# Kernel tuning notes

Hardware: AMD Instinct MI355X
Metric: run time of the kernel (lower is better)

Reference implementation:

```python
import jax, jax.numpy as jnp
import numpy as np
from jax import lax

CLASSES = 6
R = 8            # zoom_factor
FEAT = 32        # DUC loops i,j in range(32)
OUT_PAD = 304    # DUC hardcodes zeros(b,6,304,304)
IMG = 256        # original image H=W -> final bilinear resize target
BN_EPS = 1e-5
DN = ('NCHW', 'OIHW', 'NCHW')


def _duc(x):
    # x: [B, classes*r*r, H', W'] ; original loop only reads top-left 32x32
    x = x[:, :, :FEAT, :FEAT]
    B = x.shape[0]
    # channel order in original: view(b, classes, r*r) -> (classes, r, r)
    y = x.reshape(B, CLASSES, R, R, FEAT, FEAT)
    y = y.transpose(0, 1, 4, 2, 5, 3).reshape(B, CLASSES, FEAT * R, FEAT * R)  # [B,6,256,256]
    pad = OUT_PAD - FEAT * R
    return jnp.pad(y, ((0, 0), (0, 0), (0, pad), (0, pad)))  # zeros ring like torch.zeros buffer


def _bilinear_align_corners(x, oh, ow):
    b, c, h, w = x.shape
    ys = jnp.linspace(0.0, h - 1.0, oh)
    xs = jnp.linspace(0.0, w - 1.0, ow)
    y0 = jnp.floor(ys).astype(jnp.int32)
    x0 = jnp.floor(xs).astype(jnp.int32)
    y1 = jnp.minimum(y0 + 1, h - 1)
    x1 = jnp.minimum(x0 + 1, w - 1)
    wy = (ys - y0)[None, None, :, None]
    wx = (xs - x0)[None, None, None, :]
    rows = x[:, :, y0, :] * (1.0 - wy) + x[:, :, y1, :] * wy          # [b,c,oh,w]
    out = rows[:, :, :, x0] * (1.0 - wx) + rows[:, :, :, x1] * wx     # [b,c,oh,ow]
    return out


def setup_inputs() -> dict:
    key = jax.random.key(0)
    ks = jax.random.split(key, 8)
    x = jax.random.normal(ks[0], (16, 5632, 32, 32), jnp.float32)
    w1 = jax.random.normal(ks[1], (512, 5632, 1, 1), jnp.float32) * 0.02
    gamma = 1.0 + 0.1 * jax.random.normal(ks[2], (512,), jnp.float32)
    beta = 0.1 * jax.random.normal(ks[3], (512,), jnp.float32)
    mean = 0.1 * jax.random.normal(ks[4], (512,), jnp.float32)
    var = jax.random.uniform(ks[5], (512,), jnp.float32, 0.5, 1.5)
    w2 = jax.random.normal(ks[6], (CLASSES * R * R, 512, 1, 1), jnp.float32) * 0.02
    b2 = jax.random.normal(ks[7], (CLASSES * R * R,), jnp.float32) * 0.02
    return {'x': x, 'w1': w1, 'gamma': gamma, 'beta': beta, 'mean': mean, 'var': var, 'w2': w2, 'b2': b2}


def reference(x, w1, gamma, beta, mean, var, w2, b2):
    # cls head: 1x1 conv with padding=1 (quirk in source) -> 34x34 map
    h = lax.conv_general_dilated(x, w1, (1, 1), ((1, 1), (1, 1)), dimension_numbers=DN)
    inv = lax.rsqrt(var + BN_EPS)
    h = (h - mean[None, :, None, None]) * (inv * gamma)[None, :, None, None] + beta[None, :, None, None]
    h = jax.nn.relu(h)  # Dropout2d is identity at inference
    h = lax.conv_general_dilated(h, w2, (1, 1), ((0, 0), (0, 0)), dimension_numbers=DN)
    h = h + b2[None, :, None, None]            # [B,384,34,34]
    h = _duc(h)                                # [B,6,304,304]
    h = jax.nn.softmax(h, axis=1)
    return _bilinear_align_corners(h, IMG, IMG)  # [B,6,256,256]
```

## Files before the change

### kernel.cpp

```cpp
#include <hip/hip_runtime.h>
#include <hip/hip_bf16.h>
#include <stdint.h>

typedef float f32x4 __attribute__((ext_vector_type(4)));
typedef short s16x8 __attribute__((ext_vector_type(8)));
typedef unsigned short u16;

__device__ __forceinline__ u16 f2bf(float f) {
  uint32_t u = __float_as_uint(f);
  u = (u + 0x7fffu + ((u >> 16) & 1u)) >> 16;
  return (u16)u;
}

__global__ void k_params(const float* __restrict__ gamma, const float* __restrict__ beta,
                         const float* __restrict__ mean, const float* __restrict__ var,
                         float* __restrict__ bnS, float* __restrict__ bnT) {
  int i = threadIdx.x;
  if (i < 512) {
    float s = gamma[i] * rsqrtf(var[i] + 1e-5f);
    bnS[i] = s;
    bnT[i] = beta[i] - mean[i] * s;
  }
}

__global__ void k_convert(const float* __restrict__ in, u16* __restrict__ out, int n4) {
  int i = blockIdx.x * blockDim.x + threadIdx.x;
  if (i < n4) {
    float4 v = ((const float4*)in)[i];
    ushort4 o;
    o.x = f2bf(v.x); o.y = f2bf(v.y); o.z = f2bf(v.z); o.w = f2bf(v.w);
    ((ushort4*)out)[i] = o;
  }
}

__global__ void k_border2(const float* __restrict__ w2, const float* __restrict__ b2,
                          const float* __restrict__ bnT, float* __restrict__ border2) {
  int o = blockIdx.x;
  int l = threadIdx.x;
  float s = 0.f;
  for (int j = 0; j < 8; ++j) {
    int c = l + 64 * j;
    s += w2[o * 512 + c] * fmaxf(bnT[c], 0.f);
  }
  for (int off = 32; off > 0; off >>= 1) s += __shfl_down(s, off, 64);
  if (l == 0) border2[o] = s + b2[o];
}

__global__ __launch_bounds__(256, 2) void k_gemm1(
    const float* __restrict__ X, const u16* __restrict__ B,
    const float* __restrict__ bnS, const float* __restrict__ bnT,
    u16* __restrict__ H) {
  const int K = 5632;
  __shared__ __align__(16) u16 sA[128 * 40];
  __shared__ __align__(16) u16 sB[4096];
  int nb = gridDim.x;
  int id = blockIdx.x;
  int li = (id & 7) * (nb >> 3) + (id >> 3);
  int nt = li & 3;
  int mt = li >> 2;
  int t = threadIdx.x;
  int l = t & 63, w = t >> 6;
  int wm = w >> 1, wn = w & 1;

  auto swz = [](int u) { int m = u >> 2, g = u & 3; return (m * 4 + (g ^ ((m >> 1) & 3))) * 8; };
  int wo0 = swz(t), wo1 = swz(t + 256);

  int m0 = (w >> 1) * 64 + 2 * (l & 31);
  int kh = w & 1;
  int kq = l >> 5;
  int bidx = mt >> 3, p0 = (mt & 7) * 128;
  const float* gA = X + (size_t)bidx * (5632ull * 1024) + (size_t)(kh * 16 + kq * 8) * 1024
                      + p0 + m0;
  int aoff = m0 * 40 + kh * 16 + kq * 8;

  const u16* gB0 = B + (size_t)(nt * 128 + (t >> 2)) * K + (t & 3) * 8;
  const u16* gB1 = gB0 + (size_t)64 * K;

  int offA[4], offB[4];
#pragma unroll
  for (int f = 0; f < 4; ++f) {
    int m = wm * 64 + f * 16 + (l & 15);
    offA[f] = m * 40 + (l >> 4) * 8;
    int n = wn * 64 + f * 16 + (l & 15);
    int g = l >> 4;
    offB[f] = (n * 4 + (g ^ ((n >> 1) & 3))) * 8;
  }

  f32x4 acc[4][4] = {};

  float2 va[8];
  s16x8 rB0, rB1;
#pragma unroll
  for (int i = 0; i < 8; ++i) va[i] = *(const float2*)(gA + (size_t)i * 1024);
  rB0 = *(const s16x8*)gB0;
  rB1 = *(const s16x8*)gB1;

  for (int k0 = 0; k0 < K; k0 += 32) {
    union { u16 u[16]; s16x8 v[2]; } cv;
#pragma unroll
    for (int i = 0; i < 8; ++i) {
      cv.u[i] = f2bf(va[i].x);
      cv.u[8 + i] = f2bf(va[i].y);
    }
    *(s16x8*)(sA + aoff) = cv.v[0];
    *(s16x8*)(sA + aoff + 40) = cv.v[1];
    *(s16x8*)(sB + wo0) = rB0;
    *(s16x8*)(sB + wo1) = rB1;
    __syncthreads();
    if (k0 + 32 < K) {
      gA += 32 * 1024;
      gB0 += 32; gB1 += 32;
#pragma unroll
      for (int i = 0; i < 8; ++i) va[i] = *(const float2*)(gA + (size_t)i * 1024);
      rB0 = *(const s16x8*)gB0;
      rB1 = *(const s16x8*)gB1;
    }
    s16x8 af[4], bf[4];
#pragma unroll
    for (int f = 0; f < 4; ++f) {
      af[f] = *(const s16x8*)(sA + offA[f]);
      bf[f] = *(const s16x8*)(sB + offB[f]);
    }
#pragma unroll
    for (int i = 0; i < 4; ++i)
#pragma unroll
      for (int j = 0; j < 4; ++j)
        acc[i][j] = __builtin_amdgcn_mfma_f32_16x16x32_bf16(af[i], bf[j], acc[i][j], 0, 0, 0);
    __syncthreads();
  }

  int mb = mt * 128 + wm * 64;
  int nbase = nt * 128 + wn * 64;
#pragma unroll
  for (int j = 0; j < 4; ++j) {
    int n_g = nbase + j * 16 + (l & 15);
    float s = bnS[n_g], tt = bnT[n_g];
#pragma unroll
    for (int i = 0; i < 4; ++i)
#pragma unroll
      for (int r = 0; r < 4; ++r) {
        int m_g = mb + i * 16 + (l >> 4) * 4 + r;
        float v = fmaxf(acc[i][j][r] * s + tt, 0.f);
        H[(size_t)m_g * 512 + n_g] = f2bf(v);
      }
  }
}

__global__ __launch_bounds__(256, 2) void k_gemm2(
    const u16* __restrict__ A, const u16* __restrict__ B,
    const float* __restrict__ b2, float* __restrict__ C) {
  const int K = 512;
  __shared__ __align__(16) u16 sA[4096];
  __shared__ __align__(16) u16 sB[4096];
  int nb = gridDim.x;
  int id = blockIdx.x;
  int li = (id & 7) * (nb >> 3) + (id >> 3);
  int nt = li % 3;
  int mt = li / 3;
  int t = threadIdx.x;
  int l = t & 63, w = t >> 6;
  int wm = w >> 1, wn = w & 1;

  auto swz = [](int u) { int m = u >> 2, g = u & 3; return (m * 4 + (g ^ ((m >> 1) & 3))) * 8; };
  int wo0 = swz(t), wo1 = swz(t + 256);

  const u16* gA0 = A + (size_t)(mt * 128 + (t >> 2)) * K + (t & 3) * 8;
  const u16* gA1 = gA0 + (size_t)64 * K;
  const u16* gB0 = B + (size_t)(nt * 128 + (t >> 2)) * K + (t & 3) * 8;
  const u16* gB1 = gB0 + (size_t)64 * K;

  int offA[4], offB[4];
#pragma unroll
  for (int f = 0; f < 4; ++f) {
    int g = l >> 4;
    int m = wm * 64 + f * 16 + (l & 15);
    offA[f] = (m * 4 + (g ^ ((m >> 1) & 3))) * 8;
    int n = wn * 64 + f * 16 + (l & 15);
    offB[f] = (n * 4 + (g ^ ((n >> 1) & 3))) * 8;
  }

  f32x4 acc[4][4] = {};

  s16x8 rA0 = *(const s16x8*)gA0;
  s16x8 rA1 = *(const s16x8*)gA1;
  s16x8 rB0 = *(const s16x8*)gB0;
  s16x8 rB1 = *(const s16x8*)gB1;

  for (int k0 = 0; k0 < K; k0 += 32) {
    *(s16x8*)(sA + wo0) = rA0;
    *(s16x8*)(sA + wo1) = rA1;
    *(s16x8*)(sB + wo0) = rB0;
    *(s16x8*)(sB + wo1) = rB1;
    __syncthreads();
    if (k0 + 32 < K) {
      gA0 += 32; gA1 += 32; gB0 += 32; gB1 += 32;
      rA0 = *(const s16x8*)gA0;
      rA1 = *(const s16x8*)gA1;
      rB0 = *(const s16x8*)gB0;
      rB1 = *(const s16x8*)gB1;
    }
    s16x8 af[4], bf[4];
#pragma unroll
    for (int f = 0; f < 4; ++f) {
      af[f] = *(const s16x8*)(sA + offA[f]);
      bf[f] = *(const s16x8*)(sB + offB[f]);
    }
#pragma unroll
    for (int i = 0; i < 4; ++i)
#pragma unroll
      for (int j = 0; j < 4; ++j)
        acc[i][j] = __builtin_amdgcn_mfma_f32_16x16x32_bf16(af[i], bf[j], acc[i][j], 0, 0, 0);
    __syncthreads();
  }

  int mb = mt * 128 + wm * 64;
  int nbase = nt * 128 + wn * 64;
#pragma unroll
  for (int j = 0; j < 4; ++j) {
    int n_g = nbase + j * 16 + (l & 15);
    float bias = b2[n_g];
#pragma unroll
    for (int i = 0; i < 4; ++i)
#pragma unroll
      for (int r = 0; r < 4; ++r) {
        int m_g = mb + i * 16 + (l >> 4) * 4 + r;
        C[(size_t)m_g * 384 + n_g] = acc[i][j][r] + bias;
      }
  }
}

__global__ __launch_bounds__(256) void k_out(const float* __restrict__ c2,
                                             const float* __restrict__ border2,
                                             float* __restrict__ out) {
  int b = blockIdx.x >> 8;
  int oy = blockIdx.x & 255;
  int ox = threadIdx.x;
  const float SCL = 303.0f / 255.0f;
  float ys = oy * SCL, xs = ox * SCL;
  int y0 = (int)ys; if (y0 > 303) y0 = 303;
  int x0 = (int)xs; if (x0 > 303) x0 = 303;
  float wy = ys - (float)y0, wx = xs - (float)x0;
  int y1 = y0 + 1; if (y1 > 303) y1 = 303;
  int x1 = x0 + 1; if (x1 > 303) x1 = 303;
  int syA[2] = {y0, y1};
  int sxA[2] = {x0, x1};
  float wyA[2] = {1.f - wy, wy};
  float wxA[2] = {1.f - wx, wx};
  float acc[6] = {0.f, 0.f, 0.f, 0.f, 0.f, 0.f};
#pragma unroll
  for (int cy = 0; cy < 2; ++cy) {
#pragma unroll
    for (int cx = 0; cx < 2; ++cx) {
      float wgt = wyA[cy] * wxA[cx];
      int sy = syA[cy], sx = sxA[cx];
      if (sy >= 256 || sx >= 256) {
        float p = wgt * (1.f / 6.f);
#pragma unroll
        for (int c = 0; c < 6; ++c) acc[c] += p;
      } else {
        int i = sy >> 3, j = sx >> 3;
        int sub = ((sy & 7) << 3) | (sx & 7);
        const float* src;
        if (i == 0 || j == 0)
          src = border2 + sub;
        else
          src = c2 + (size_t)((b << 10) + ((i - 1) << 5) + (j - 1)) * 384 + sub;
        float l0 = src[0],   l1 = src[64],  l2 = src[128];
        float l3 = src[192], l4 = src[256], l5 = src[320];
        float mx = fmaxf(fmaxf(fmaxf(l0, l1), fmaxf(l2, l3)), fmaxf(l4, l5));
        float e0 = __expf(l0 - mx), e1 = __expf(l1 - mx), e2 = __expf(l2 - mx);
        float e3 = __expf(l3 - mx), e4 = __expf(l4 - mx), e5 = __expf(l5 - mx);
        float ssum = e0 + e1 + e2 + e3 + e4 + e5;
        float r = wgt / ssum;
        acc[0] += e0 * r; acc[1] += e1 * r; acc[2] += e2 * r;
        acc[3] += e3 * r; acc[4] += e4 * r; acc[5] += e5 * r;
      }
    }
  }
  size_t base = ((size_t)b * 6) << 16;
  int pix = (oy << 8) | ox;
#pragma unroll
  for (int c = 0; c < 6; ++c) out[base + ((size_t)c << 16) + pix] = acc[c];
}

extern "C" void kernel_launch(void* const* d_in, const int* in_sizes, int n_in,
                              void* d_out, int out_size, void* d_ws, size_t ws_size,
                              hipStream_t stream) {
  const float* x     = (const float*)d_in[0];
  const float* w1    = (const float*)d_in[1];
  const float* gamma = (const float*)d_in[2];
  const float* beta  = (const float*)d_in[3];
  const float* mean  = (const float*)d_in[4];
  const float* var   = (const float*)d_in[5];
  const float* w2    = (const float*)d_in[6];
  const float* b2    = (const float*)d_in[7];
  float* out = (float*)d_out;

  char* ws = (char*)d_ws;
  size_t off = 0;
  auto alloc = [&](size_t bytes) -> char* {
    char* p = ws + off;
    off = (off + bytes + 255) & ~(size_t)255;
    return p;
  };
  u16*   w1bf    = (u16*)alloc(512ull * 5632 * 2);
  u16*   w2bf    = (u16*)alloc(384ull * 512 * 2);
  float* bnS     = (float*)alloc(512 * 4);
  float* bnT     = (float*)alloc(512 * 4);
  float* border2 = (float*)alloc(384 * 4);
  u16*   h       = (u16*)alloc(16384ull * 512 * 2);
  float* c2      = (float*)alloc(16384ull * 384 * 4);
  (void)ws_size;

  k_params<<<dim3(1), dim3(512), 0, stream>>>(gamma, beta, mean, var, bnS, bnT);
  k_convert<<<dim3(2816), dim3(256), 0, stream>>>(w1, w1bf, 512 * 5632 / 4);
  k_convert<<<dim3(192), dim3(256), 0, stream>>>(w2, w2bf, 384 * 512 / 4);
  k_border2<<<dim3(384), dim3(64), 0, stream>>>(w2, b2, bnT, border2);

  k_gemm1<<<dim3(512), dim3(256), 0, stream>>>(x, w1bf, bnS, bnT, h);
  k_gemm2<<<dim3(128 * 3), dim3(256), 0, stream>>>(h, w2bf, b2, c2);
  k_out<<<dim3(16 * 256), dim3(256), 0, stream>>>(c2, border2, out);
}
```

Baseline: 260.5 us.

## Double-buffer LDS in gemm1 and shrink N tile to 64 for more blocks

Rewrites the first GEMM's main loop to use two LDS stages so the next tile's global loads and bf16 conversion overlap with MFMA compute on the current tile. The N tile drops from 128 to 64, so each wave computes a 32x64 sub-tile, the grid doubles to 1024 blocks, and launch bounds allow 3 blocks per CU. This trades more redundant reads and conversion of the fp32 X tile, since each X tile is now converted by twice as many blocks, for better latency hiding and occupancy.

```diff
diff --git a/kernel.cpp b/kernel.cpp
--- a/kernel.cpp
+++ b/kernel.cpp
@@ -46,97 +46,105 @@
   if (l == 0) border2[o] = s + b2[o];
 }
 
-__global__ __launch_bounds__(256, 2) void k_gemm1(
-    const float* __restrict__ X, const u16* __restrict__ B,
+__global__ __launch_bounds__(256, 3) void k_gemm1(
+    const float* __restrict__ X, const u16* __restrict__ Bw,
     const float* __restrict__ bnS, const float* __restrict__ bnT,
     u16* __restrict__ H) {
   const int K = 5632;
-  __shared__ __align__(16) u16 sA[128 * 40];
-  __shared__ __align__(16) u16 sB[4096];
+  const int NT = 176;
+  __shared__ __align__(16) u16 sA[2][128 * 40];
+  __shared__ __align__(16) u16 sB[2][64 * 32];
   int nb = gridDim.x;
   int id = blockIdx.x;
   int li = (id & 7) * (nb >> 3) + (id >> 3);
-  int nt = li & 3;
-  int mt = li >> 2;
+  int nt = li & 7;
+  int mt = li >> 3;
   int t = threadIdx.x;
   int l = t & 63, w = t >> 6;
-  int wm = w >> 1, wn = w & 1;
-
-  auto swz = [](int u) { int m = u >> 2, g = u & 3; return (m * 4 + (g ^ ((m >> 1) & 3))) * 8; };
-  int wo0 = swz(t), wo1 = swz(t + 256);
+
+  const u16* gB = Bw + (size_t)(nt * 64 + (t >> 2)) * K + (t & 3) * 8;
+  int woB;
+  { int n = t >> 2, g = t & 3; woB = (n * 4 + (g ^ ((n >> 1) & 3))) * 8; }
 
   int m0 = (w >> 1) * 64 + 2 * (l & 31);
-  int kh = w & 1;
-  int kq = l >> 5;
+  int kh = w & 1, kq = l >> 5;
   int bidx = mt >> 3, p0 = (mt & 7) * 128;
   const float* gA = X + (size_t)bidx * (5632ull * 1024) + (size_t)(kh * 16 + kq * 8) * 1024
                       + p0 + m0;
   int aoff = m0 * 40 + kh * 16 + kq * 8;
 
-  const u16* gB0 = B + (size_t)(nt * 128 + (t >> 2)) * K + (t & 3) * 8;
-  const u16* gB1 = gB0 + (size_t)64 * K;
-
-  int offA[4], offB[4];
+  int offA[2], offB[4];
+#pragma unroll
+  for (int f = 0; f < 2; ++f) offA[f] = (w * 32 + f * 16 + (l & 15)) * 40 + (l >> 4) * 8;
 #pragma unroll
   for (int f = 0; f < 4; ++f) {
-    int m = wm * 64 + f * 16 + (l & 15);
-    offA[f] = m * 40 + (l >> 4) * 8;
-    int n = wn * 64 + f * 16 + (l & 15);
-    int g = l >> 4;
+    int n = f * 16 + (l & 15), g = l >> 4;
     offB[f] = (n * 4 + (g ^ ((n >> 1) & 3))) * 8;
   }
 
-  f32x4 acc[4][4] = {};
-
-  float2 va[8];
-  s16x8 rB0, rB1;
-#pragma unroll
-  for (int i = 0; i < 8; ++i) va[i] = *(const float2*)(gA + (size_t)i * 1024);
-  rB0 = *(const s16x8*)gB0;
-  rB1 = *(const s16x8*)gB1;
-
-  for (int k0 = 0; k0 < K; k0 += 32) {
+  f32x4 acc[2][4] = {};
+
+  auto loadA = [&](float2* va) {
+#pragma unroll
+    for (int ii = 0; ii < 8; ++ii) va[ii] = *(const float2*)(gA + (size_t)ii * 1024);
+  };
+  auto stage = [&](const float2* va, s16x8 rB, u16* bA, u16* bB) {
     union { u16 u[16]; s16x8 v[2]; } cv;
 #pragma unroll
-    for (int i = 0; i < 8; ++i) {
-      cv.u[i] = f2bf(va[i].x);
-      cv.u[8 + i] = f2bf(va[i].y);
-    }
-    *(s16x8*)(sA + aoff) = cv.v[0];
-    *(s16x8*)(sA + aoff + 40) = cv.v[1];
-    *(s16x8*)(sB + wo0) = rB0;
-    *(s16x8*)(sB + wo1) = rB1;
+    for (int ii = 0; ii < 8; ++ii) {
+      cv.u[ii] = f2bf(va[ii].x);
+      cv.u[8 + ii] = f2bf(va[ii].y);
+    }
+    *(s16x8*)(bA + aoff) = cv.v[0];
+    *(s16x8*)(bA + aoff + 40) = cv.v[1];
+    *(s16x8*)(bB + woB) = rB;
+  };
+  auto compute = [&](const u16* bA, const u16* bB) {
+    s16x8 af[2], bfr[4];
+#pragma unroll
+    for (int f = 0; f < 2; ++f) af[f] = *(const s16x8*)(bA + offA[f]);
+#pragma unroll
+    for (int f = 0; f < 4; ++f) bfr[f] = *(const s16x8*)(bB + offB[f]);
+#pragma unroll
+    for (int ii = 0; ii < 2; ++ii)
+#pragma unroll
+      for (int j = 0; j < 4; ++j)
+        acc[ii][j] = __builtin_amdgcn_mfma_f32_16x16x32_bf16(af[ii], bfr[j], acc[ii][j], 0, 0, 0);
+  };
+
+  float2 vaA[8], vaB[8];
+  s16x8 rBa, rBb;
+
+  loadA(vaA); rBa = *(const s16x8*)gB;
+  stage(vaA, rBa, sA[0], sB[0]);
+  gA += 32 * 1024; gB += 32;
+  loadA(vaB); rBb = *(const s16x8*)gB;
+
+  for (int i = 0; i < NT; i += 2) {
     __syncthreads();
-    if (k0 + 32 < K) {
-      gA += 32 * 1024;
-      gB0 += 32; gB1 += 32;
-#pragma unroll
-      for (int i = 0; i < 8; ++i) va[i] = *(const float2*)(gA + (size_t)i * 1024);
-      rB0 = *(const s16x8*)gB0;
-      rB1 = *(const s16x8*)gB1;
-    }
-    s16x8 af[4], bf[4];
-#pragma unroll
-    for (int f = 0; f < 4; ++f) {
-      af[f] = *(const s16x8*)(sA + offA[f]);
-      bf[f] = *(const s16x8*)(sB + offB[f]);
-    }
-#pragma unroll
-    for (int i = 0; i < 4; ++i)
-#pragma unroll
-      for (int j = 0; j < 4; ++j)
-        acc[i][j] = __builtin_amdgcn_mfma_f32_16x16x32_bf16(af[i], bf[j], acc[i][j], 0, 0, 0);
+    if (i + 2 < NT) {
+      gA += 32 * 1024; gB += 32;
+      loadA(vaA); rBa = *(const s16x8*)gB;
+    }
+    compute(sA[0], sB[0]);
+    stage(vaB, rBb, sA[1], sB[1]);
     __syncthreads();
-  }
-
-  int mb = mt * 128 + wm * 64;
-  int nbase = nt * 128 + wn * 64;
+    if (i + 3 < NT) {
+      gA += 32 * 1024; gB += 32;
+      loadA(vaB); rBb = *(const s16x8*)gB;
+    }
+    compute(sA[1], sB[1]);
+    if (i + 2 < NT) stage(vaA, rBa, sA[0], sB[0]);
+  }
+
+  int mb = mt * 128 + w * 32;
+  int nb0 = nt * 64;
 #pragma unroll
   for (int j = 0; j < 4; ++j) {
-    int n_g = nbase + j * 16 + (l & 15);
+    int n_g = nb0 + j * 16 + (l & 15);
     float s = bnS[n_g], tt = bnT[n_g];
 #pragma unroll
-    for (int i = 0; i < 4; ++i)
+    for (int i = 0; i < 2; ++i)
 #pragma unroll
       for (int r = 0; r < 4; ++r) {
         int m_g = mb + i * 16 + (l >> 4) * 4 + r;
@@ -317,7 +325,7 @@
   k_convert<<<dim3(192), dim3(256), 0, stream>>>(w2, w2bf, 384 * 512 / 4);
   k_border2<<<dim3(384), dim3(64), 0, stream>>>(w2, b2, bnT, border2);
 
-  k_gemm1<<<dim3(512), dim3(256), 0, stream>>>(x, w1bf, bnS, bnT, h);
+  k_gemm1<<<dim3(1024), dim3(256), 0, stream>>>(x, w1bf, bnS, bnT, h);
   k_gemm2<<<dim3(128 * 3), dim3(256), 0, stream>>>(h, w2bf, b2, c2);
   k_out<<<dim3(16 * 256), dim3(256), 0, stream>>>(c2, border2, out);
 }
```

Result: slower. 340.5 us (+30.7%).

## Double-buffer LDS in GEMM1 with two-deep register prefetch and one barrier per stage

Applied to the files above, without the earlier changes.

The main 1x1-conv GEMM now keeps two LDS buffers for A and B and two register sets of prefetched global data. Each half-iteration computes on one buffer while the next tile is converted and written into the other, so only one barrier is needed per k-step instead of two. The manual bf16 rounding is also replaced by the HIP __float2bfloat16 intrinsic. LDS usage doubles and more registers are held live, which may reduce occupancy under the 2-blocks launch bound.

```diff
diff --git a/kernel.cpp b/kernel.cpp
--- a/kernel.cpp
+++ b/kernel.cpp
@@ -10,6 +10,12 @@
   uint32_t u = __float_as_uint(f);
   u = (u + 0x7fffu + ((u >> 16) & 1u)) >> 16;
   return (u16)u;
+}
+
+__device__ __forceinline__ u16 cvt_bf(float f) {
+  union { __hip_bfloat16 h; u16 u; } c;
+  c.h = __float2bfloat16(f);
+  return c.u;
 }
 
 __global__ void k_params(const float* __restrict__ gamma, const float* __restrict__ beta,
@@ -47,12 +53,13 @@
 }
 
 __global__ __launch_bounds__(256, 2) void k_gemm1(
-    const float* __restrict__ X, const u16* __restrict__ B,
+    const float* __restrict__ X, const u16* __restrict__ Bw,
     const float* __restrict__ bnS, const float* __restrict__ bnT,
     u16* __restrict__ H) {
   const int K = 5632;
-  __shared__ __align__(16) u16 sA[128 * 40];
-  __shared__ __align__(16) u16 sB[4096];
+  const int NT = 176;
+  __shared__ __align__(16) u16 sA[2][128 * 40];
+  __shared__ __align__(16) u16 sB[2][4096];
   int nb = gridDim.x;
   int id = blockIdx.x;
   int li = (id & 7) * (nb >> 3) + (id >> 3);
@@ -64,17 +71,15 @@
 
   auto swz = [](int u) { int m = u >> 2, g = u & 3; return (m * 4 + (g ^ ((m >> 1) & 3))) * 8; };
   int wo0 = swz(t), wo1 = swz(t + 256);
+  const u16* gB0 = Bw + (size_t)(nt * 128 + (t >> 2)) * K + (t & 3) * 8;
+  const u16* gB1 = gB0 + (size_t)64 * K;
 
   int m0 = (w >> 1) * 64 + 2 * (l & 31);
-  int kh = w & 1;
-  int kq = l >> 5;
+  int kh = w & 1, kq = l >> 5;
   int bidx = mt >> 3, p0 = (mt & 7) * 128;
   const float* gA = X + (size_t)bidx * (5632ull * 1024) + (size_t)(kh * 16 + kq * 8) * 1024
                       + p0 + m0;
   int aoff = m0 * 40 + kh * 16 + kq * 8;
-
-  const u16* gB0 = B + (size_t)(nt * 128 + (t >> 2)) * K + (t & 3) * 8;
-  const u16* gB1 = gB0 + (size_t)64 * K;
 
   int offA[4], offB[4];
 #pragma unroll
@@ -88,45 +93,59 @@
 
   f32x4 acc[4][4] = {};
 
-  float2 va[8];
-  s16x8 rB0, rB1;
-#pragma unroll
-  for (int i = 0; i < 8; ++i) va[i] = *(const float2*)(gA + (size_t)i * 1024);
-  rB0 = *(const s16x8*)gB0;
-  rB1 = *(const s16x8*)gB1;
-
-  for (int k0 = 0; k0 < K; k0 += 32) {
+  auto loadA = [&](float2* va) {
+#pragma unroll
+    for (int ii = 0; ii < 8; ++ii) va[ii] = *(const float2*)(gA + (size_t)ii * 1024);
+  };
+  auto stage = [&](const float2* va, s16x8 r0, s16x8 r1, u16* bA, u16* bB) {
     union { u16 u[16]; s16x8 v[2]; } cv;
 #pragma unroll
-    for (int i = 0; i < 8; ++i) {
-      cv.u[i] = f2bf(va[i].x);
-      cv.u[8 + i] = f2bf(va[i].y);
-    }
-    *(s16x8*)(sA + aoff) = cv.v[0];
-    *(s16x8*)(sA + aoff + 40) = cv.v[1];
-    *(s16x8*)(sB + wo0) = rB0;
-    *(s16x8*)(sB + wo1) = rB1;
+    for (int ii = 0; ii < 8; ++ii) {
+      cv.u[ii] = cvt_bf(va[ii].x);
+      cv.u[8 + ii] = cvt_bf(va[ii].y);
+    }
+    *(s16x8*)(bA + aoff) = cv.v[0];
+    *(s16x8*)(bA + aoff + 40) = cv.v[1];
+    *(s16x8*)(bB + wo0) = r0;
+    *(s16x8*)(bB + wo1) = r1;
+  };
+  auto compute = [&](const u16* bA, const u16* bB) {
+    s16x8 af[4], bfr[4];
+#pragma unroll
+    for (int f = 0; f < 4; ++f) {
+      af[f] = *(const s16x8*)(bA + offA[f]);
+      bfr[f] = *(const s16x8*)(bB + offB[f]);
+    }
+#pragma unroll
+    for (int ii = 0; ii < 4; ++ii)
+#pragma unroll
+      for (int j = 0; j < 4; ++j)
+        acc[ii][j] = __builtin_amdgcn_mfma_f32_16x16x32_bf16(af[ii], bfr[j], acc[ii][j], 0, 0, 0);
+  };
+
+  float2 vaA[8], vaB[8];
+  s16x8 rBa0, rBa1, rBb0, rBb1;
+
+  loadA(vaA); rBa0 = *(const s16x8*)gB0; rBa1 = *(const s16x8*)gB1;
+  stage(vaA, rBa0, rBa1, sA[0], sB[0]);
+  gA += 32 * 1024; gB0 += 32; gB1 += 32;
+  loadA(vaB); rBb0 = *(const s16x8*)gB0; rBb1 = *(const s16x8*)gB1;
+
+  for (int i = 0; i < NT; i += 2) {
     __syncthreads();
-    if (k0 + 32 < K) {
-      gA += 32 * 1024;
-      gB0 += 32; gB1 += 32;
-#pragma unroll
-      for (int i = 0; i < 8; ++i) va[i] = *(const float2*)(gA + (size_t)i * 1024);
-      rB0 = *(const s16x8*)gB0;
-      rB1 = *(const s16x8*)gB1;
-    }
-    s16x8 af[4], bf[4];
-#pragma unroll
-    for (int f = 0; f < 4; ++f) {
-      af[f] = *(const s16x8*)(sA + offA[f]);
-      bf[f] = *(const s16x8*)(sB + offB[f]);
-    }
-#pragma unroll
-    for (int i = 0; i < 4; ++i)
-#pragma unroll
-      for (int j = 0; j < 4; ++j)
-        acc[i][j] = __builtin_amdgcn_mfma_f32_16x16x32_bf16(af[i], bf[j], acc[i][j], 0, 0, 0);
+    if (i + 2 < NT) {
+      gA += 32 * 1024; gB0 += 32; gB1 += 32;
+      loadA(vaA); rBa0 = *(const s16x8*)gB0; rBa1 = *(const s16x8*)gB1;
+    }
+    compute(sA[0], sB[0]);
+    stage(vaB, rBb0, rBb1, sA[1], sB[1]);
     __syncthreads();
+    if (i + 3 < NT) {
+      gA += 32 * 1024; gB0 += 32; gB1 += 32;
+      loadA(vaB); rBb0 = *(const s16x8*)gB0; rBb1 = *(const s16x8*)gB1;
+    }
+    compute(sA[1], sB[1]);
+    if (i + 2 < NT) stage(vaA, rBa0, rBa1, sA[0], sB[0]);
   }
 
   int mb = mt * 128 + wm * 64;
```

New measurement: 265.2 us. About the same (+1.8%).
